# Kernel optimization log

Measured on AMD Instinct MI355X. Metric: run time of the kernel, lower is better.

## Reference

```python
import jax, jax.numpy as jnp
import numpy as np

BITS = 50

def _xor(a, b):
    # binary XOR on {0,1} floats: a + b - 2ab
    return a + b - 2.0 * a * b

def _maj(a, b, c):
    # majority (carry-out of a full adder) on {0,1} floats
    return a * b + a * c + b * c - 2.0 * a * b * c

def setup_inputs() -> dict:
    key = jax.random.key(0)
    kA, kB = jax.random.split(key)
    N = 1_000_000
    A = jax.random.randint(kA, (N, BITS), 0, 2).astype(jnp.float32)
    B = jax.random.randint(kB, (N, BITS), 0, 2).astype(jnp.float32)
    return {"A": A, "B": B}

def reference(A, B):
    """A - B via two's complement ripple-carry: A + NOT(B) + 1, LSB first.
    Returns (result [..., 50], borrow [..., 1])."""
    not_b = 1.0 - B                      # VecNOT
    # scan over the 50 bits (sequential carry dependency)
    a_bits = jnp.moveaxis(A, -1, 0)      # [50, N]
    b_bits = jnp.moveaxis(not_b, -1, 0)  # [50, N]
    c0 = jnp.ones(A.shape[:-1], dtype=A.dtype)  # initial carry = 1

    def step(c, ab):
        a, b = ab
        s = _xor(_xor(a, b), c)          # FullAdder sum
        c_next = _maj(a, b, c)           # FullAdder carry
        return c_next, s

    c_final, sums = jax.lax.scan(step, c0, (a_bits, b_bits))
    result = jnp.moveaxis(sums, 0, -1)   # [N, 50]
    borrow = (1.0 - c_final)[..., None]  # borrow_not(carry), [N, 1]
    return result, borrow
```

## Files before the change

kernel.cpp:

```cpp
#include <hip/hip_runtime.h>


constexpr int BITS = 50;
constexpr unsigned long long MASK50 = (1ULL << BITS) - 1ULL;

__device__ inline unsigned long long shfl64(unsigned long long v, int src) {
    int lo = __shfl((int)(unsigned)(v & 0xffffffffULL), src, 64);
    int hi = __shfl((int)(unsigned)(v >> 32), src, 64);
    return ((unsigned long long)(unsigned)hi << 32) | (unsigned long long)(unsigned)lo;
}

__global__ __launch_bounds__(256) void Subtractor50Bit_kernel(
    const float* __restrict__ A, const float* __restrict__ B,
    float* __restrict__ out, int N)
{
    const int lane = threadIdx.x & 63;
    const int wv   = threadIdx.x >> 6;
    const long long waveIdx = (long long)blockIdx.x * 4 + wv;
    const long long rowBase = waveIdx * 64;
    if (rowBase >= N) return;

    if (rowBase + 64 <= N) {
        const long long eBase = rowBase * BITS;
        const int p0   = BITS * lane;
        const int idx0 = p0 >> 6;
        const int sh   = p0 & 63;

        unsigned long long a0 = 0, a1 = 0, b0 = 0, b1 = 0;
        #pragma unroll
        for (int j = 0; j < BITS; ++j) {
            float va = A[eBase + j * 64 + lane];
            unsigned long long m = __ballot(va != 0.0f);
            if (j == idx0)     a0 = m;
            if (j == idx0 + 1) a1 = m;
        }
        #pragma unroll
        for (int j = 0; j < BITS; ++j) {
            float vb = B[eBase + j * 64 + lane];
            unsigned long long m = __ballot(vb != 0.0f);
            if (j == idx0)     b0 = m;
            if (j == idx0 + 1) b1 = m;
        }

        unsigned long long av = a0 >> sh;
        unsigned long long bv = b0 >> sh;
        if (sh > 64 - BITS) {
            av |= a1 << (64 - sh);
            bv |= b1 << (64 - sh);
        }
        av &= MASK50;
        bv &= MASK50;

        unsigned long long diff = (av - bv) & MASK50;
        float borrow = (av < bv) ? 1.0f : 0.0f;

        #pragma unroll
        for (int j = 0; j < BITS; ++j) {
            int local = j * 64 + lane;
            int r     = local / BITS;
            int bit   = local - r * BITS;
            unsigned long long dr = shfl64(diff, r);
            out[eBase + local] = (float)((dr >> bit) & 1ULL);
        }
        out[(long long)N * BITS + rowBase + lane] = borrow;
    } else {
        long long r = rowBase + lane;
        if (r < N) {
            unsigned long long av = 0, bv = 0;
            for (int k = 0; k < BITS; ++k) {
                av |= (unsigned long long)(A[r * BITS + k] != 0.0f) << k;
                bv |= (unsigned long long)(B[r * BITS + k] != 0.0f) << k;
            }
            unsigned long long diff = (av - bv) & MASK50;
            for (int k = 0; k < BITS; ++k)
                out[r * BITS + k] = (float)((diff >> k) & 1ULL);
            out[(long long)N * BITS + r] = (av < bv) ? 1.0f : 0.0f;
        }
    }
}

extern "C" void kernel_launch(void* const* d_in, const int* in_sizes, int n_in,
                              void* d_out, int out_size, void* d_ws, size_t ws_size,
                              hipStream_t stream) {
    const float* A = (const float*)d_in[0];
    const float* B = (const float*)d_in[1];
    float* out = (float*)d_out;
    const int N = in_sizes[0] / BITS;

    const int waves  = (N + 63) / 64;
    const int blocks = (waves + 3) / 4;
    Subtractor50Bit_kernel<<<blocks, 256, 0, stream>>>(A, B, out, N);
}
```

Measured before the change: 538.4 us.

## Stage tiles through LDS with float4 loads and stores instead of ballot/shuffle

Each wave now loads its 64-row tile of A and B with vectorized float4 reads, transposes it through a per-wave LDS buffer to pack bits per row, and writes the output back through LDS with float4 stores. This replaces the previous 100 scalar loads with ballots and 50 shuffle-based scalar stores per wave. Bits are pulled from the float exponent bit, which assumes the inputs are exactly 0.0 or 1.0. The cost is 50 KB of LDS per block, block-wide syncs, and duplicate clamped work for out-of-range waves.

```diff
diff --git a/kernel.cpp b/kernel.cpp
--- a/kernel.cpp
+++ b/kernel.cpp
@@ -3,79 +3,127 @@
 
 constexpr int BITS = 50;
 constexpr unsigned long long MASK50 = (1ULL << BITS) - 1ULL;
+constexpr int TR = 64;
+constexpr int TE = TR * BITS;
 
-__device__ inline unsigned long long shfl64(unsigned long long v, int src) {
-    int lo = __shfl((int)(unsigned)(v & 0xffffffffULL), src, 64);
-    int hi = __shfl((int)(unsigned)(v >> 32), src, 64);
-    return ((unsigned long long)(unsigned)hi << 32) | (unsigned long long)(unsigned)lo;
-}
-
-__global__ __launch_bounds__(256) void Subtractor50Bit_kernel(
+__global__ __launch_bounds__(256, 3) void Subtractor50Bit_kernel(
     const float* __restrict__ A, const float* __restrict__ B,
-    float* __restrict__ out, int N)
+    float* __restrict__ out, int N, int numTiles)
 {
+    __shared__ float buf[4][TE];
     const int lane = threadIdx.x & 63;
     const int wv   = threadIdx.x >> 6;
-    const long long waveIdx = (long long)blockIdx.x * 4 + wv;
-    const long long rowBase = waveIdx * 64;
-    if (rowBase >= N) return;
 
-    if (rowBase + 64 <= N) {
-        const long long eBase = rowBase * BITS;
-        const int p0   = BITS * lane;
-        const int idx0 = p0 >> 6;
-        const int sh   = p0 & 63;
-
-        unsigned long long a0 = 0, a1 = 0, b0 = 0, b1 = 0;
-        #pragma unroll
-        for (int j = 0; j < BITS; ++j) {
-            float va = A[eBase + j * 64 + lane];
-            unsigned long long m = __ballot(va != 0.0f);
-            if (j == idx0)     a0 = m;
-            if (j == idx0 + 1) a1 = m;
-        }
-        #pragma unroll
-        for (int j = 0; j < BITS; ++j) {
-            float vb = B[eBase + j * 64 + lane];
-            unsigned long long m = __ballot(vb != 0.0f);
-            if (j == idx0)     b0 = m;
-            if (j == idx0 + 1) b1 = m;
-        }
-
-        unsigned long long av = a0 >> sh;
-        unsigned long long bv = b0 >> sh;
-        if (sh > 64 - BITS) {
-            av |= a1 << (64 - sh);
-            bv |= b1 << (64 - sh);
-        }
-        av &= MASK50;
-        bv &= MASK50;
-
-        unsigned long long diff = (av - bv) & MASK50;
-        float borrow = (av < bv) ? 1.0f : 0.0f;
-
-        #pragma unroll
-        for (int j = 0; j < BITS; ++j) {
-            int local = j * 64 + lane;
-            int r     = local / BITS;
-            int bit   = local - r * BITS;
-            unsigned long long dr = shfl64(diff, r);
-            out[eBase + local] = (float)((dr >> bit) & 1ULL);
-        }
-        out[(long long)N * BITS + rowBase + lane] = borrow;
-    } else {
-        long long r = rowBase + lane;
+    if (blockIdx.x == 0 && threadIdx.x < 64) {
+        long long r = (long long)numTiles * TR + lane;
         if (r < N) {
             unsigned long long av = 0, bv = 0;
             for (int k = 0; k < BITS; ++k) {
                 av |= (unsigned long long)(A[r * BITS + k] != 0.0f) << k;
                 bv |= (unsigned long long)(B[r * BITS + k] != 0.0f) << k;
             }
-            unsigned long long diff = (av - bv) & MASK50;
+            unsigned long long d = (av - bv) & MASK50;
             for (int k = 0; k < BITS; ++k)
-                out[r * BITS + k] = (float)((diff >> k) & 1ULL);
+                out[r * BITS + k] = (float)((d >> k) & 1ULL);
             out[(long long)N * BITS + r] = (av < bv) ? 1.0f : 0.0f;
         }
+    }
+
+    if (numTiles <= 0) return;
+
+    long long t = (long long)blockIdx.x * 4 + wv;
+    if (t >= numTiles) t = numTiles - 1;
+
+    float* S = buf[wv];
+    float4* S4 = (float4*)S;
+    float2* S2t = (float2*)(S + 3072);
+    const long long eBase = t * (long long)TE;
+
+    float4 ra[12], rb[12];
+    float2 ra2, rb2;
+    {
+        const float4* a4 = (const float4*)(A + eBase);
+        const float4* b4 = (const float4*)(B + eBase);
+        #pragma unroll
+        for (int k = 0; k < 12; ++k) {
+            ra[k] = a4[k * 64 + lane];
+            rb[k] = b4[k * 64 + lane];
+        }
+        ra2 = ((const float2*)(A + eBase + 3072))[lane];
+        rb2 = ((const float2*)(B + eBase + 3072))[lane];
+    }
+
+    #pragma unroll
+    for (int k = 0; k < 12; ++k) S4[k * 64 + lane] = ra[k];
+    S2t[lane] = ra2;
+    __syncthreads();
+
+    unsigned long long av;
+    {
+        const float2* R = (const float2*)(S + BITS * lane);
+        unsigned int lo = 0, hi = 0;
+        #pragma unroll
+        for (int k = 0; k < 25; ++k) {
+            float2 v = R[k];
+            unsigned int b0 = (__float_as_uint(v.x) >> 29) & 1u;
+            unsigned int b1 = (__float_as_uint(v.y) >> 29) & 1u;
+            const int j = 2 * k;
+            if (j < 32)     lo |= b0 << j;        else hi |= b0 << (j - 32);
+            if (j + 1 < 32) lo |= b1 << (j + 1);  else hi |= b1 << (j + 1 - 32);
+        }
+        av = ((unsigned long long)hi << 32) | lo;
+    }
+    __syncthreads();
+
+    #pragma unroll
+    for (int k = 0; k < 12; ++k) S4[k * 64 + lane] = rb[k];
+    S2t[lane] = rb2;
+    __syncthreads();
+
+    unsigned long long bv;
+    {
+        const float2* R = (const float2*)(S + BITS * lane);
+        unsigned int lo = 0, hi = 0;
+        #pragma unroll
+        for (int k = 0; k < 25; ++k) {
+            float2 v = R[k];
+            unsigned int b0 = (__float_as_uint(v.x) >> 29) & 1u;
+            unsigned int b1 = (__float_as_uint(v.y) >> 29) & 1u;
+            const int j = 2 * k;
+            if (j < 32)     lo |= b0 << j;        else hi |= b0 << (j - 32);
+            if (j + 1 < 32) lo |= b1 << (j + 1);  else hi |= b1 << (j + 1 - 32);
+        }
+        bv = ((unsigned long long)hi << 32) | lo;
+    }
+    __syncthreads();
+
+    const unsigned long long diff = (av - bv) & MASK50;
+    const float borrow = (av < bv) ? 1.0f : 0.0f;
+    const unsigned int dlo = (unsigned int)diff;
+    const unsigned int dhi = (unsigned int)(diff >> 32);
+
+    {
+        float2* W = (float2*)(S + BITS * lane);
+        #pragma unroll
+        for (int k = 0; k < 25; ++k) {
+            const int j = 2 * k;
+            unsigned int b0 = ((j < 32) ? (dlo >> j) : (dhi >> (j - 32))) & 1u;
+            unsigned int b1 = ((j + 1 < 32) ? (dlo >> (j + 1)) : (dhi >> (j + 1 - 32))) & 1u;
+            W[k] = make_float2((float)b0, (float)b1);
+        }
+    }
+    __syncthreads();
+
+    {
+        float4* o4 = (float4*)(out + eBase);
+        #pragma unroll
+        for (int k = 0; k < 12; ++k) {
+            float4 v = S4[k * 64 + lane];
+            o4[k * 64 + lane] = v;
+        }
+        float2 v2 = S2t[lane];
+        ((float2*)(out + eBase + 3072))[lane] = v2;
+        out[(long long)N * BITS + t * TR + lane] = borrow;
     }
 }
 
@@ -87,7 +135,8 @@
     float* out = (float*)d_out;
     const int N = in_sizes[0] / BITS;
 
-    const int waves  = (N + 63) / 64;
-    const int blocks = (waves + 3) / 4;
-    Subtractor50Bit_kernel<<<blocks, 256, 0, stream>>>(A, B, out, N);
+    const int numTiles = N / TR;
+    int blocks = (numTiles + 3) / 4;
+    if (blocks < 1) blocks = 1;
+    Subtractor50Bit_kernel<<<blocks, 256, 0, stream>>>(A, B, out, N, numTiles);
 }
```

Result: faster. 477.2 us (-11.4%).
